# Performance work log

Hardware: AMD Instinct MI355X
Metric: run time of the kernel (lower is better)

Reference implementation:

```python
import jax, jax.numpy as jnp
import numpy as np

IMG = 224
NUM_VIEWS = 6
K = 5  # splat kernel size (5x5 = 25 offsets)


def setup_inputs() -> dict:
    key = jax.random.key(0)
    points = jax.random.normal(key, (16, 32768, 3), dtype=jnp.float32)
    return {"points": points}


def _render(points):
    B, N, _ = points.shape
    deg2rad = jnp.pi / 180.0
    az = jnp.linspace(0.0, 360.0, NUM_VIEWS + 1)[:-1] * deg2rad          # (V,)
    el = jnp.array([0.0, 30.0, -30.0, 0.0, 0.0, 0.0])[:NUM_VIEWS] * deg2rad

    # 5x5 splat offsets in normalized coords, matching torch meshgrid(ij) + stack([dx,dy])
    off = jnp.linspace(-2.0 / IMG, 2.0 / IMG, K)
    dyg, dxg = jnp.meshgrid(off, off, indexing="ij")
    koff = jnp.stack([dxg, dyg], axis=-1).reshape(-1, 2)                  # (25, 2)

    def one_view(a, e):
        x, y, z = points[..., 0], points[..., 1], points[..., 2]
        x_rot = x * jnp.cos(a) - z * jnp.sin(a)
        z_rot = x * jnp.sin(a) + z * jnp.cos(a)
        y_rot = y * jnp.cos(e) - z_rot * jnp.sin(e)
        z_fin = y * jnp.sin(e) + z_rot * jnp.cos(e)                       # (B, N)
        p2d = jnp.stack([x_rot, y_rot], axis=-1)                          # (B, N, 2)

        zmin = jnp.min(z_fin, axis=1, keepdims=True)
        zmax = jnp.max(z_fin, axis=1, keepdims=True)
        feat = 0.3 + 0.7 * (z_fin - zmin) / (zmax - zmin + 1e-6)          # (B, N), in [0.3, 1.0]

        coords = p2d[:, :, None, :] + koff[None, None, :, :]              # (B, N, 25, 2)
        # torch .long() truncates toward zero; astype(int32) does too
        px = ((coords[..., 0] + 1.0) * 0.5 * (IMG - 1)).astype(jnp.int32)
        py = ((coords[..., 1] + 1.0) * 0.5 * (IMG - 1)).astype(jnp.int32)
        valid = (px >= 0) & (px < IMG) & (py >= 0) & (py < IMG)
        # invalid splats routed out-of-bounds and dropped by the scatter
        idx = jnp.where(valid, py * IMG + px, IMG * IMG).reshape(B, -1)   # (B, N*25)
        f = jnp.broadcast_to(feat[:, :, None], (B, N, K * K)).reshape(B, -1)

        def splat(i, fv):
            return jnp.zeros(IMG * IMG, dtype=points.dtype).at[i].max(fv, mode="drop")

        img = jax.vmap(splat)(idx, f).reshape(B, IMG, IMG)
        # all 3 channels receive the identical feature values
        return jnp.broadcast_to(img[:, None], (B, 3, IMG, IMG))

    views = jax.vmap(one_view)(az, el)                                    # (V, B, 3, H, W)
    return jnp.transpose(views, (1, 0, 2, 3, 4))                          # (B, V, 3, H, W)


def reference(points) -> jnp.ndarray:
    return _render(points)
```

## Files before the change

### kernel.cpp

```cpp
#include <hip/hip_runtime.h>
#include <math.h>

#define IMG    224
#define NVIEWS 6
#define BATCH  16
#define NPTS   32768
#define PLANE  (IMG * IMG)
#define HROWS  112
#define TILE_ELEMS (HROWS * IMG)
#define NTHREADS 1024
#define NWG (BATCH * NVIEWS * 2)

struct ViewTrig {
    float sa[NVIEWS], ca[NVIEWS], se[NVIEWS], ce[NVIEWS];
    float off0, off4;
};

__device__ __forceinline__ float fmul_(float a, float b) {
#pragma clang fp contract(off)
    return a * b;
}
__device__ __forceinline__ float fadd_(float a, float b) {
#pragma clang fp contract(off)
    return a + b;
}
__device__ __forceinline__ float fsub_(float a, float b) {
#pragma clang fp contract(off)
    return a - b;
}
__device__ __forceinline__ int pix_(float c) {
    return (int)fmul_(fmul_(fadd_(c, 1.0f), 0.5f), 223.0f);
}

__global__ __launch_bounds__(NTHREADS, 4) void render_kernel(
    const float* __restrict__ pts, float* __restrict__ out, ViewTrig vt)
{
    extern __shared__ __align__(16) int tile[];
    __shared__ float smin[NTHREADS / 64], smax[NTHREADS / 64];

    const int wg = blockIdx.x;
    const int h  = wg & 1;
    const int bv = wg >> 1;
    const int b = bv / NVIEWS, v = bv - b * NVIEWS;
    const int row0 = h * HROWS;

    const float sa = vt.sa[v], ca = vt.ca[v], se = vt.se[v], ce = vt.ce[v];
    const float* p = pts + (size_t)b * NPTS * 3;

    for (int i = threadIdx.x; i < TILE_ELEMS; i += NTHREADS) tile[i] = 0;

    float zmin = INFINITY, zmax = -INFINITY;
    for (int n = threadIdx.x; n < NPTS; n += NTHREADS) {
        const float x = p[n * 3 + 0];
        const float y = p[n * 3 + 1];
        const float z = p[n * 3 + 2];
        const float zr = fmaf(z, ca, x * sa);
        const float zf = fmaf(zr, ce, y * se);
        zmin = fminf(zmin, zf);
        zmax = fmaxf(zmax, zf);
    }
    for (int o = 32; o > 0; o >>= 1) {
        zmin = fminf(zmin, __shfl_down(zmin, o, 64));
        zmax = fmaxf(zmax, __shfl_down(zmax, o, 64));
    }
    const int wave = threadIdx.x >> 6;
    if ((threadIdx.x & 63) == 0) { smin[wave] = zmin; smax[wave] = zmax; }
    __syncthreads();
    if (threadIdx.x == 0) {
        float mn = smin[0], mx = smax[0];
        for (int w = 1; w < NTHREADS / 64; ++w) {
            mn = fminf(mn, smin[w]);
            mx = fmaxf(mx, smax[w]);
        }
        smin[0] = mn; smax[0] = mx;
    }
    __syncthreads();
    zmin = smin[0]; zmax = smax[0];
    const float scale = 0.7f / ((zmax - zmin) + 1e-6f);
    const float bias  = 0.3f - zmin * scale;
    __syncthreads();

    for (int n = threadIdx.x; n < NPTS; n += NTHREADS) {
        const float x = p[n * 3 + 0];
        const float y = p[n * 3 + 1];
        const float z = p[n * 3 + 2];

        const float zr = fadd_(fmul_(x, sa), fmul_(z, ca));
        const float yr = fsub_(fmul_(y, ce), fmul_(zr, se));
        const float xr = fsub_(fmul_(x, ca), fmul_(z, sa));

        const int y0i = max(pix_(fadd_(yr, vt.off0)), row0);
        const int y1i = min(pix_(fadd_(yr, vt.off4)), row0 + HROWS - 1);
        const int x0i = max(pix_(fadd_(xr, vt.off0)), 0);
        const int x1i = min(pix_(fadd_(xr, vt.off4)), IMG - 1);

        const float zf = fmaf(zr, ce, y * se);
        const int fb = __float_as_int(fmaf(zf, scale, bias));

        #pragma unroll
        for (int dy = 0; dy < 3; ++dy) {
            const int ry = y0i + dy;
            const bool yok = (ry <= y1i);
            const int base = (ry - row0) * IMG;
            #pragma unroll
            for (int dx = 0; dx < 3; ++dx) {
                const int cx = x0i + dx;
                if (yok && (cx <= x1i)) atomicMax(&tile[base + cx], fb);
            }
        }
    }
    __syncthreads();

    float* dst = out + ((size_t)bv * 3) * PLANE + (size_t)row0 * IMG;
    const float4* src = (const float4*)tile;
    #pragma unroll
    for (int c = 0; c < 3; ++c) {
        float4* d4 = (float4*)(dst + (size_t)c * PLANE);
        for (int i = threadIdx.x; i < TILE_ELEMS / 4; i += NTHREADS)
            d4[i] = src[i];
    }
}

extern "C" void kernel_launch(void* const* d_in, const int* in_sizes, int n_in,
                              void* d_out, int out_size, void* d_ws, size_t ws_size,
                              hipStream_t stream)
{
    const float* pts = (const float*)d_in[0];
    float* out = (float*)d_out;

    ViewTrig vt;
    const float d2r = (float)(M_PI / 180.0);
    const float el_deg[NVIEWS] = {0.0f, 30.0f, -30.0f, 0.0f, 0.0f, 0.0f};
    for (int v = 0; v < NVIEWS; ++v) {
        float a = (float)(60 * v) * d2r;
        float e = el_deg[v] * d2r;
        vt.sa[v] = (float)sin((double)a);
        vt.ca[v] = (float)cos((double)a);
        vt.se[v] = (float)sin((double)e);
        vt.ce[v] = (float)cos((double)e);
    }
    {
        const float s = (float)(2.0 / 224.0);
        vt.off0 = -s;
        vt.off4 = s;
    }

    static bool attr_set = false;
    (void)attr_set;
    hipFuncSetAttribute(reinterpret_cast<const void*>(render_kernel),
                        hipFuncAttributeMaxDynamicSharedMemorySize,
                        TILE_ELEMS * (int)sizeof(int));

    render_kernel<<<NWG, NTHREADS, TILE_ELEMS * sizeof(int), stream>>>(pts, out, vt);
}
```

Measured before the change: 105.5 us.

## Fuse min/max and splat passes by atomically maxing order-preserving raw depth

```diff
diff --git a/kernel.cpp b/kernel.cpp
--- a/kernel.cpp
+++ b/kernel.cpp
@@ -10,6 +10,8 @@
 #define TILE_ELEMS (HROWS * IMG)
 #define NTHREADS 1024
 #define NWG (BATCH * NVIEWS * 2)
+
+typedef float fx4 __attribute__((ext_vector_type(4)));
 
 struct ViewTrig {
     float sa[NVIEWS], ca[NVIEWS], se[NVIEWS], ce[NVIEWS];
@@ -32,33 +34,85 @@
     return (int)fmul_(fmul_(fadd_(c, 1.0f), 0.5f), 223.0f);
 }
 
+__device__ __forceinline__ unsigned fmap_(float f) {
+    unsigned b = __float_as_uint(f);
+    return b ^ ((unsigned)((int)b >> 31) | 0x80000000u);
+}
+__device__ __forceinline__ float fmap_inv_(unsigned u) {
+    unsigned b = (u & 0x80000000u) ? (u ^ 0x80000000u) : ~u;
+    return __uint_as_float(b);
+}
+
 __global__ __launch_bounds__(NTHREADS, 4) void render_kernel(
     const float* __restrict__ pts, float* __restrict__ out, ViewTrig vt)
 {
-    extern __shared__ __align__(16) int tile[];
+    extern __shared__ __align__(16) unsigned tile[];
     __shared__ float smin[NTHREADS / 64], smax[NTHREADS / 64];
 
-    const int wg = blockIdx.x;
-    const int h  = wg & 1;
-    const int bv = wg >> 1;
-    const int b = bv / NVIEWS, v = bv - b * NVIEWS;
+    const int bid  = blockIdx.x;
+    const int xcd  = bid & 7;
+    const int slot = bid >> 3;
+    const int hi   = (slot >= 12) ? 1 : 0;
+    const int b    = xcd + 8 * hi;
+    const int vh   = slot - 12 * hi;
+    const int v    = vh >> 1;
+    const int h    = vh & 1;
+    const int bv   = b * NVIEWS + v;
     const int row0 = h * HROWS;
 
     const float sa = vt.sa[v], ca = vt.ca[v], se = vt.se[v], ce = vt.ce[v];
-    const float* p = pts + (size_t)b * NPTS * 3;
+    const float off0 = vt.off0, off4 = vt.off4;
+    const float4* p4 = (const float4*)(pts + (size_t)b * NPTS * 3);
 
-    for (int i = threadIdx.x; i < TILE_ELEMS; i += NTHREADS) tile[i] = 0;
+    {
+        int4* t4 = (int4*)tile;
+        for (int i = threadIdx.x; i < TILE_ELEMS / 4; i += NTHREADS)
+            t4[i] = make_int4(0, 0, 0, 0);
+    }
+    __syncthreads();
 
     float zmin = INFINITY, zmax = -INFINITY;
-    for (int n = threadIdx.x; n < NPTS; n += NTHREADS) {
-        const float x = p[n * 3 + 0];
-        const float y = p[n * 3 + 1];
-        const float z = p[n * 3 + 2];
-        const float zr = fmaf(z, ca, x * sa);
+
+    auto do_point = [&](float x, float y, float z) {
+        const float zr = fadd_(fmul_(x, sa), fmul_(z, ca));
+        const float yr = fsub_(fmul_(y, ce), fmul_(zr, se));
+        const float xr = fsub_(fmul_(x, ca), fmul_(z, sa));
+
+        const int y0i = max(pix_(fadd_(yr, off0)), row0);
+        const int y1i = min(pix_(fadd_(yr, off4)), row0 + HROWS - 1);
+        const int x0i = max(pix_(fadd_(xr, off0)), 0);
+        const int x1i = min(pix_(fadd_(xr, off4)), IMG - 1);
+
         const float zf = fmaf(zr, ce, y * se);
         zmin = fminf(zmin, zf);
         zmax = fmaxf(zmax, zf);
+        const unsigned fz = fmap_(zf);
+
+        #pragma unroll
+        for (int dy = 0; dy < 3; ++dy) {
+            const int ry = y0i + dy;
+            const bool yok = (ry <= y1i);
+            const int base = (ry - row0) * IMG;
+            #pragma unroll
+            for (int dx = 0; dx < 3; ++dx) {
+                const int cx = x0i + dx;
+                if (yok && (cx <= x1i)) atomicMax(&tile[base + cx], fz);
+            }
+        }
+    };
+
+    #pragma unroll
+    for (int k = 0; k < NPTS / (4 * NTHREADS); ++k) {
+        const int g = threadIdx.x + k * NTHREADS;
+        const float4 A = p4[3 * g + 0];
+        const float4 B = p4[3 * g + 1];
+        const float4 C = p4[3 * g + 2];
+        do_point(A.x, A.y, A.z);
+        do_point(A.w, B.x, B.y);
+        do_point(B.z, B.w, C.x);
+        do_point(C.y, C.z, C.w);
     }
+
     for (int o = 32; o > 0; o >>= 1) {
         zmin = fminf(zmin, __shfl_down(zmin, o, 64));
         zmax = fmaxf(zmax, __shfl_down(zmax, o, 64));
@@ -75,49 +129,21 @@
         smin[0] = mn; smax[0] = mx;
     }
     __syncthreads();
-    zmin = smin[0]; zmax = smax[0];
-    const float scale = 0.7f / ((zmax - zmin) + 1e-6f);
-    const float bias  = 0.3f - zmin * scale;
-    __syncthreads();
-
-    for (int n = threadIdx.x; n < NPTS; n += NTHREADS) {
-        const float x = p[n * 3 + 0];
-        const float y = p[n * 3 + 1];
-        const float z = p[n * 3 + 2];
-
-        const float zr = fadd_(fmul_(x, sa), fmul_(z, ca));
-        const float yr = fsub_(fmul_(y, ce), fmul_(zr, se));
-        const float xr = fsub_(fmul_(x, ca), fmul_(z, sa));
-
-        const int y0i = max(pix_(fadd_(yr, vt.off0)), row0);
-        const int y1i = min(pix_(fadd_(yr, vt.off4)), row0 + HROWS - 1);
-        const int x0i = max(pix_(fadd_(xr, vt.off0)), 0);
-        const int x1i = min(pix_(fadd_(xr, vt.off4)), IMG - 1);
-
-        const float zf = fmaf(zr, ce, y * se);
-        const int fb = __float_as_int(fmaf(zf, scale, bias));
-
-        #pragma unroll
-        for (int dy = 0; dy < 3; ++dy) {
-            const int ry = y0i + dy;
-            const bool yok = (ry <= y1i);
-            const int base = (ry - row0) * IMG;
-            #pragma unroll
-            for (int dx = 0; dx < 3; ++dx) {
-                const int cx = x0i + dx;
-                if (yok && (cx <= x1i)) atomicMax(&tile[base + cx], fb);
-            }
-        }
-    }
-    __syncthreads();
+    const float scale = 0.7f / ((smax[0] - smin[0]) + 1e-6f);
+    const float bias  = 0.3f - smin[0] * scale;
 
     float* dst = out + ((size_t)bv * 3) * PLANE + (size_t)row0 * IMG;
-    const float4* src = (const float4*)tile;
-    #pragma unroll
-    for (int c = 0; c < 3; ++c) {
-        float4* d4 = (float4*)(dst + (size_t)c * PLANE);
-        for (int i = threadIdx.x; i < TILE_ELEMS / 4; i += NTHREADS)
-            d4[i] = src[i];
+    const uint4* src = (const uint4*)tile;
+    for (int i = threadIdx.x; i < TILE_ELEMS / 4; i += NTHREADS) {
+        const uint4 u = src[i];
+        fx4 f;
+        f.x = (u.x == 0u) ? 0.0f : fmaf(fmap_inv_(u.x), scale, bias);
+        f.y = (u.y == 0u) ? 0.0f : fmaf(fmap_inv_(u.y), scale, bias);
+        f.z = (u.z == 0u) ? 0.0f : fmaf(fmap_inv_(u.z), scale, bias);
+        f.w = (u.w == 0u) ? 0.0f : fmaf(fmap_inv_(u.w), scale, bias);
+        #pragma unroll
+        for (int c = 0; c < 3; ++c)
+            __builtin_nontemporal_store(f, (fx4*)(dst + (size_t)c * PLANE) + i);
     }
 }
 
@@ -145,11 +171,9 @@
         vt.off4 = s;
     }
 
-    static bool attr_set = false;
-    (void)attr_set;
-    hipFuncSetAttribute(reinterpret_cast<const void*>(render_kernel),
-                        hipFuncAttributeMaxDynamicSharedMemorySize,
-                        TILE_ELEMS * (int)sizeof(int));
+    (void)hipFuncSetAttribute(reinterpret_cast<const void*>(render_kernel),
+                              hipFuncAttributeMaxDynamicSharedMemorySize,
+                              TILE_ELEMS * (int)sizeof(int));
 
     render_kernel<<<NWG, NTHREADS, TILE_ELEMS * sizeof(int), stream>>>(pts, out, vt);
 }
```

New measurement: 91.54 us. 13.3% less time.
